# Optimization experiments

Hardware: AMD Instinct MI355X
Metric: run time of the kernel (lower is better)

The kernel has to match this reference:

```python
import jax, jax.numpy as jnp
import numpy as np

B, T, E, H = 8, 2048, 1024, 64  # batch, seq_len(=block_size), embedding_size, head_size


def setup_inputs() -> dict:
    key = jax.random.key(0)
    k1, k2, k3, k4, k5 = jax.random.split(key, 5)
    x = jax.random.normal(k1, (B, T, E), dtype=jnp.float32)
    Wk = jax.random.normal(k2, (H, E), dtype=jnp.float32) * 0.02
    Wq = jax.random.normal(k3, (H, E), dtype=jnp.float32) * 0.02
    Wv = jax.random.normal(k4, (H, E), dtype=jnp.float32) * 0.02
    attention_mask = jax.random.randint(k5, (B, T), 0, 2).astype(jnp.int32)
    return {"x": x, "Wk": Wk, "Wq": Wq, "Wv": Wv, "attention_mask": attention_mask}


def reference(x, Wk, Wq, Wv, attention_mask):
    # Linear projections (nn.Linear with no bias: y = x @ W.T)
    k = jnp.einsum('bte,he->bth', x, Wk)
    q = jnp.einsum('bte,he->bth', x, Wq)
    v = jnp.einsum('bte,he->bth', x, Wv)
    scale = v.shape[2] ** -0.5  # head_size^-0.5, faithful to v.shape[2]**(-0.5)
    wei = jnp.einsum('bqh,bkh->bqk', q, k) * scale  # [B,T,T]
    # Causal mask (tril buffer) AND padding outer-product mask; the double-precision
    # outer product in the original just tests nonzero-ness, so a boolean AND is exact.
    causal = jnp.tril(jnp.ones((T, T), dtype=bool))  # [T,T]
    pad = (attention_mask[:, :, None] * attention_mask[:, None, :]) != 0  # [B,T,T]
    wei = jnp.where(causal[None, :, :] & pad, wei, -jnp.inf)
    wei = jax.nn.softmax(wei, axis=-1)
    wei = jnp.nan_to_num(wei)  # fully-masked rows -> 0 (matches torch.nan_to_num)
    # dropout in eval mode -> identity
    out = jnp.einsum('bqk,bkh->bqh', wei, v)
    return out
```

## Files before the change

### kernel.cpp

```cpp
#include <hip/hip_runtime.h>
#include <hip/hip_bf16.h>

typedef __bf16 bf16x8 __attribute__((ext_vector_type(8)));
typedef __bf16 bf16x4 __attribute__((ext_vector_type(4)));
typedef float  f32x4  __attribute__((ext_vector_type(4)));

#define LDP  72
#define KLDP 72
#define VLDP 72
#define PLDP 72

#define BAR() { asm volatile("s_waitcnt lgkmcnt(0)" ::: "memory"); __builtin_amdgcn_s_barrier(); }

__global__ __launch_bounds__(256) void wconv_kernel(
    const float* __restrict__ Wk, const float* __restrict__ Wq,
    const float* __restrict__ Wv, const int* __restrict__ mask,
    __bf16* __restrict__ wbf, unsigned* __restrict__ maskw)
{
    if (blockIdx.x == 192) {
        for (int wdx = threadIdx.x; wdx < 512; wdx += 256) {
            unsigned wv = 0;
            #pragma unroll
            for (int bit = 0; bit < 32; bit++)
                wv |= (mask[wdx * 32 + bit] != 0 ? 1u : 0u) << bit;
            maskw[wdx] = wv;
        }
        return;
    }
    int idx = blockIdx.x * 256 + threadIdx.x;
    int row = idx >> 8;
    int c4  = idx & 255;
    const float* wp = (row < 64) ? Wk + (size_t)row * 1024
                    : (row < 128) ? Wq + (size_t)(row - 64) * 1024
                                  : Wv + (size_t)(row - 128) * 1024;
    float4 f = *reinterpret_cast<const float4*>(wp + c4 * 4);
    bf16x4 v; v[0] = (__bf16)f.x; v[1] = (__bf16)f.y; v[2] = (__bf16)f.z; v[3] = (__bf16)f.w;
    *reinterpret_cast<bf16x4*>(&wbf[(size_t)row * 1024 + c4 * 4]) = v;
}

__global__ __launch_bounds__(1024) void proj_kernel(
    const float* __restrict__ x, const __bf16* __restrict__ wbf,
    __bf16* __restrict__ kbuf, __bf16* __restrict__ qbuf, __bf16* __restrict__ vtbuf)
{
    __shared__ __align__(16) __bf16 Slds[2][256 * LDP];
    __shared__ __align__(16) __bf16 Vtl[64 * LDP];

    const int tid  = threadIdx.x;
    const int lane = tid & 63;
    const int wid  = tid >> 6;
    const int wm   = wid >> 2;
    const int wn   = wid & 3;
    const int mbase = blockIdx.x * 64;

    const int cl = lane & 15;
    const int e0 = (lane >> 4) * 8;
    const int r0 = (lane >> 4) * 4;

    const int arow = tid >> 4, acg = tid & 15;
    const float* aptr = x + (size_t)(mbase + arow) * 1024 + acg * 4;

    float4 a0, a1;
    bf16x4 w0[3], w1[3];

#define ISSUE(aset, wset, kb) { \
    aset = *reinterpret_cast<const float4*>(aptr + (kb)); \
    _Pragma("unroll") \
    for (int i_ = 0; i_ < 3; i_++) { \
        int c_ = i_ * 1024 + tid; \
        wset[i_] = *reinterpret_cast<const bf16x4*>(&wbf[(size_t)(c_ >> 4) * 1024 + (kb) + (c_ & 15) * 4]); \
    } }

#define COMMIT(aset, wset, bufi) { \
    bf16x4 av_; \
    av_[0] = (__bf16)aset.x; av_[1] = (__bf16)aset.y; av_[2] = (__bf16)aset.z; av_[3] = (__bf16)aset.w; \
    *reinterpret_cast<bf16x4*>(&Slds[bufi][arow * LDP + acg * 4]) = av_; \
    _Pragma("unroll") \
    for (int i_ = 0; i_ < 3; i_++) { \
        int c_ = i_ * 1024 + tid; \
        *reinterpret_cast<bf16x4*>(&Slds[bufi][(64 + (c_ >> 4)) * LDP + (c_ & 15) * 4]) = wset[i_]; \
    } }

    f32x4 acc[3];
    #pragma unroll
    for (int n = 0; n < 3; n++) acc[n] = (f32x4){0.f, 0.f, 0.f, 0.f};

    ISSUE(a0, w0, 0);
    COMMIT(a0, w0, 0);
    ISSUE(a1, w1, 64);
    BAR();

    #pragma unroll 2
    for (int j = 0; j < 16; j++) {
        if (j < 14) {
            if (j & 1) { ISSUE(a1, w1, (j + 2) * 64); }
            else       { ISSUE(a0, w0, (j + 2) * 64); }
        }
        const __bf16* buf = Slds[j & 1];
        #pragma unroll
        for (int kk = 0; kk < 2; kk++) {
            bf16x8 a = *reinterpret_cast<const bf16x8*>(&buf[(wm * 16 + cl) * LDP + kk * 32 + e0]);
            #pragma unroll
            for (int nf = 0; nf < 3; nf++) {
                bf16x8 b = *reinterpret_cast<const bf16x8*>(&buf[(64 + wn * 48 + nf * 16 + cl) * LDP + kk * 32 + e0]);
                acc[nf] = __builtin_amdgcn_mfma_f32_16x16x32_bf16(a, b, acc[nf], 0, 0, 0);
            }
        }
        if (j < 15) {
            if (j & 1) { COMMIT(a0, w0, 0); }
            else       { COMMIT(a1, w1, 1); }
            BAR();
        }
    }
#undef ISSUE
#undef COMMIT

    #pragma unroll
    for (int nf = 0; nf < 3; nf++) {
        int c = wn * 48 + nf * 16 + cl;
        #pragma unroll
        for (int r = 0; r < 4; r++) {
            int mrel = wm * 16 + r0 + r;
            float v = acc[nf][r];
            if (c < 64)        kbuf[(size_t)(mbase + mrel) * 64 + c]         = (__bf16)v;
            else if (c < 128)  qbuf[(size_t)(mbase + mrel) * 64 + (c - 64)]  = (__bf16)v;
            else               Vtl[(c - 128) * LDP + mrel]                   = (__bf16)v;
        }
    }
    __syncthreads();
    {
        int b   = mbase >> 11;
        int tof = mbase & 2047;
        int h   = tid >> 4;
        int seg = tid & 15;
        bf16x4 v4 = *reinterpret_cast<const bf16x4*>(&Vtl[h * LDP + seg * 4]);
        *reinterpret_cast<bf16x4*>(&vtbuf[(size_t)b * 64 * 2048 + (size_t)h * 2048 + tof + seg * 4]) = v4;
    }
}

__global__ __launch_bounds__(128) void attn_kernel(
    const __bf16* __restrict__ qbuf, const __bf16* __restrict__ kbuf,
    const __bf16* __restrict__ vtbuf, const unsigned* __restrict__ maskw,
    float* __restrict__ out, float* __restrict__ accpart, float* __restrict__ mlpart,
    int nsplit, int tps)
{
    __shared__ __align__(16) __bf16 Klds[64 * KLDP];
    __shared__ __align__(16) __bf16 Vlds[64 * VLDP];
    __shared__ __align__(16) __bf16 Plds[2][2][16 * PLDP];

    const int tid  = threadIdx.x;
    const int lane = tid & 63;
    const int w    = tid >> 6;
    const int wg   = blockIdx.x;
    const int b    = wg & 7;
    const int rr_  = wg >> 3;
    const int qt   = rr_ & 31;
    const int sp   = rr_ >> 5;

    const int jbeg = sp * tps;
    const int jend = min((sp + 1) * tps, qt + 1);

    if (nsplit > 1 && jbeg >= jend) {
        for (int i = tid; i < 64; i += 128) {
            size_t mo = ((size_t)(b * nsplit + sp) * 2048 + qt * 64 + i) * 2;
            mlpart[mo] = -INFINITY; mlpart[mo + 1] = 0.f;
        }
        return;
    }

    const int cl = lane & 15;
    const int e0 = (lane >> 4) * 8;
    const int r0 = (lane >> 4) * 4;
    const int qs0 = qt * 64 + w * 16 + cl;
    const int qs1 = qs0 + 32;

    bf16x8 aq0[2], aq1[2];
    #pragma unroll
    for (int kk = 0; kk < 2; kk++) {
        aq0[kk] = *reinterpret_cast<const bf16x8*>(&qbuf[((size_t)b * 2048 + qs0) * 64 + kk * 32 + e0]);
        aq1[kk] = *reinterpret_cast<const bf16x8*>(&qbuf[((size_t)b * 2048 + qs1) * 64 + kk * 32 + e0]);
    }

    float m0 = -INFINITY, l0 = 0.f, m1 = -INFINITY, l1 = 0.f;
    f32x4 acc0[4], acc1[4];
    #pragma unroll
    for (int hf = 0; hf < 4; hf++) { acc0[hf] = (f32x4){0.f,0.f,0.f,0.f}; acc1[hf] = (f32x4){0.f,0.f,0.f,0.f}; }

    const __bf16* kb  = kbuf  + (size_t)b * 2048 * 64;
    const __bf16* vtb = vtbuf + (size_t)b * 64 * 2048;

    const int srow = tid >> 1;
    const int sc   = (tid & 1) * 32;
    bf16x8 stk[4], stv[4];

#define KV_ISSUE(jj) { _Pragma("unroll") for (int i_ = 0; i_ < 4; i_++) { \
    stk[i_] = *reinterpret_cast<const bf16x8*>(&kb[(size_t)((jj) * 64 + srow) * 64 + sc + i_ * 8]); \
    stv[i_] = *reinterpret_cast<const bf16x8*>(&vtb[(size_t)srow * 2048 + (jj) * 64 + sc + i_ * 8]); } }

#define KV_COMMIT() { _Pragma("unroll") for (int i_ = 0; i_ < 4; i_++) { \
    *reinterpret_cast<bf16x8*>(&Klds[srow * KLDP + sc + i_ * 8]) = stk[i_]; \
    *reinterpret_cast<bf16x8*>(&Vlds[srow * VLDP + sc + i_ * 8]) = stv[i_]; } }

#define SOFTMAX(S, mS, lS, accS, qsS, su) { \
    float tmax = -INFINITY; \
    _Pragma("unroll") for (int jf = 0; jf < 4; jf++) { \
        unsigned mw = (jf < 2) ? mw0 : mw1; \
        _Pragma("unroll") for (int r = 0; r < 4; r++) { \
            int kvl = jf * 16 + r0 + r; \
            bool ok = ((mw >> (kvl & 31)) & 1u) && (j * 64 + kvl <= qsS); \
            float sv = S[jf][r] * 0.125f; \
            sv = ok ? sv : -INFINITY; \
            S[jf][r] = sv; tmax = fmaxf(tmax, sv); } } \
    tmax = fmaxf(tmax, __shfl_xor(tmax, 16)); \
    tmax = fmaxf(tmax, __shfl_xor(tmax, 32)); \
    float mn = fmaxf(mS, tmax); \
    float alpha = (mn == -INFINITY) ? 1.0f : __expf(mS - mn); \
    float rs = 0.f; \
    _Pragma("unroll") for (int jf = 0; jf < 4; jf++) \
        _Pragma("unroll") for (int r = 0; r < 4; r++) { \
            float p = (mn == -INFINITY) ? 0.f : __expf(S[jf][r] - mn); \
            S[jf][r] = p; rs += p; } \
    rs += __shfl_xor(rs, 16); \
    rs += __shfl_xor(rs, 32); \
    lS = lS * alpha + rs; mS = mn; \
    _Pragma("unroll") for (int hf = 0; hf < 4; hf++) \
        _Pragma("unroll") for (int r = 0; r < 4; r++) accS[hf][r] *= alpha; \
    _Pragma("unroll") for (int jf = 0; jf < 4; jf++) { \
        bf16x4 p4; \
        _Pragma("unroll") for (int r = 0; r < 4; r++) p4[r] = (__bf16)S[jf][r]; \
        *reinterpret_cast<bf16x4*>(&Plds[w][su][cl * PLDP + jf * 16 + r0]) = p4; } }

    const int nt = jend - jbeg;
    KV_ISSUE(jbeg);
    KV_COMMIT();
    if (nt > 1) KV_ISSUE(jbeg + 1);
    BAR();

    for (int t = 0; t < nt; t++) {
        const int j = jbeg + t;

        f32x4 s0[4], s1[4];
        #pragma unroll
        for (int jf = 0; jf < 4; jf++) {
            f32x4 t0 = (f32x4){0.f,0.f,0.f,0.f}, t1 = (f32x4){0.f,0.f,0.f,0.f};
            #pragma unroll
            for (int kk = 0; kk < 2; kk++) {
                bf16x8 bk = *reinterpret_cast<const bf16x8*>(&Klds[(jf * 16 + cl) * KLDP + kk * 32 + e0]);
                t0 = __builtin_amdgcn_mfma_f32_16x16x32_bf16(bk, aq0[kk], t0, 0, 0, 0);
                t1 = __builtin_amdgcn_mfma_f32_16x16x32_bf16(bk, aq1[kk], t1, 0, 0, 0);
            }
            s0[jf] = t0; s1[jf] = t1;
        }

        const unsigned mw0 = maskw[b * 64 + j * 2];
        const unsigned mw1 = maskw[b * 64 + j * 2 + 1];
        SOFTMAX(s0, m0, l0, acc0, qs0, 0);
        SOFTMAX(s1, m1, l1, acc1, qs1, 1);

        #pragma unroll
        for (int kk = 0; kk < 2; kk++) {
            bf16x8 p0 = *reinterpret_cast<const bf16x8*>(&Plds[w][0][cl * PLDP + kk * 32 + e0]);
            bf16x8 p1 = *reinterpret_cast<const bf16x8*>(&Plds[w][1][cl * PLDP + kk * 32 + e0]);
            #pragma unroll
            for (int hf = 0; hf < 4; hf++) {
                bf16x8 av = *reinterpret_cast<const bf16x8*>(&Vlds[(hf * 16 + cl) * VLDP + kk * 32 + e0]);
                acc0[hf] = __builtin_amdgcn_mfma_f32_16x16x32_bf16(av, p0, acc0[hf], 0, 0, 0);
                acc1[hf] = __builtin_amdgcn_mfma_f32_16x16x32_bf16(av, p1, acc1[hf], 0, 0, 0);
            }
        }

        BAR();
        if (t + 1 < nt) {
            KV_COMMIT();
            if (t + 2 < nt) KV_ISSUE(j + 2);
            BAR();
        }
    }
#undef KV_ISSUE
#undef KV_COMMIT
#undef SOFTMAX

    const bool mq0 = (maskw[b * 64 + (qs0 >> 5)] >> (qs0 & 31)) & 1u;
    const bool mq1 = (maskw[b * 64 + (qs1 >> 5)] >> (qs1 & 31)) & 1u;
    if (nsplit == 1) {
        #pragma unroll
        for (int hf = 0; hf < 4; hf++)
            #pragma unroll
            for (int r = 0; r < 4; r++) {
                float v0 = (l0 > 0.f && mq0) ? acc0[hf][r] / l0 : 0.f;
                float v1 = (l1 > 0.f && mq1) ? acc1[hf][r] / l1 : 0.f;
                out[((size_t)b * 2048 + qs0) * 64 + hf * 16 + r0 + r] = v0;
                out[((size_t)b * 2048 + qs1) * 64 + hf * 16 + r0 + r] = v1;
            }
    } else {
        #pragma unroll
        for (int hf = 0; hf < 4; hf++)
            #pragma unroll
            for (int r = 0; r < 4; r++) {
                accpart[((size_t)(b * nsplit + sp) * 2048 + qs0) * 64 + hf * 16 + r0 + r] = acc0[hf][r];
                accpart[((size_t)(b * nsplit + sp) * 2048 + qs1) * 64 + hf * 16 + r0 + r] = acc1[hf][r];
            }
        if (lane < 16) {
            size_t mo0 = ((size_t)(b * nsplit + sp) * 2048 + qs0) * 2;
            size_t mo1 = ((size_t)(b * nsplit + sp) * 2048 + qs1) * 2;
            mlpart[mo0] = m0; mlpart[mo0 + 1] = l0;
            mlpart[mo1] = m1; mlpart[mo1 + 1] = l1;
        }
    }
}

template<int NS>
__global__ __launch_bounds__(256) void combine_kernel(
    const float* __restrict__ accpart, const float* __restrict__ mlpart,
    const unsigned* __restrict__ maskw, float* __restrict__ out)
{
    int idx = blockIdx.x * 256 + threadIdx.x;
    int qglob = idx >> 6;
    int h = idx & 63;
    int b = qglob >> 11;
    int qrow = qglob & 2047;

    if (!((maskw[b * 64 + (qrow >> 5)] >> (qrow & 31)) & 1u)) { out[idx] = 0.f; return; }

    float m_s[NS], l_s[NS];
    float M = -INFINITY;
    #pragma unroll
    for (int s = 0; s < NS; s++) {
        size_t mo = ((size_t)(b * NS + s) * 2048 + qrow) * 2;
        m_s[s] = mlpart[mo];
        l_s[s] = mlpart[mo + 1];
        M = fmaxf(M, m_s[s]);
    }
    if (M == -INFINITY) { out[idx] = 0.f; return; }

    float L = 0.f, O = 0.f;
    #pragma unroll
    for (int s = 0; s < NS; s++) {
        float wgt = (m_s[s] == -INFINITY) ? 0.f : __expf(m_s[s] - M);
        L += l_s[s] * wgt;
        O += wgt * accpart[((size_t)(b * NS + s) * 2048 + qrow) * 64 + h];
    }
    out[idx] = (L > 0.f) ? O / L : 0.f;
}

extern "C" void kernel_launch(void* const* d_in, const int* in_sizes, int n_in,
                              void* d_out, int out_size, void* d_ws, size_t ws_size,
                              hipStream_t stream) {
    const float* x  = (const float*)d_in[0];
    const float* Wk = (const float*)d_in[1];
    const float* Wq = (const float*)d_in[2];
    const float* Wv = (const float*)d_in[3];
    const int* mask = (const int*)d_in[4];
    float* out = (float*)d_out;

    const size_t NTOK = 8 * 2048;
    __bf16* kbuf  = (__bf16*)d_ws;
    __bf16* qbuf  = kbuf + NTOK * 64;
    __bf16* vtbuf = qbuf + NTOK * 64;
    __bf16* wbf   = vtbuf + (size_t)8 * 64 * 2048;
    unsigned* maskw = (unsigned*)(wbf + (size_t)192 * 1024);
    const size_t base_bytes = NTOK * 64 * 2 * 2 + (size_t)8 * 64 * 2048 * 2
                            + (size_t)192 * 1024 * 2 + 512 * 4;

    const size_t acc_per_split = NTOK * 64 * 4;
    const size_t ml_per_split  = NTOK * 2 * 4;
    int nsplit = 1;
    if (ws_size >= base_bytes + 4 * (acc_per_split + ml_per_split))      nsplit = 4;
    else if (ws_size >= base_bytes + 2 * (acc_per_split + ml_per_split)) nsplit = 2;

    float* accpart = (float*)((char*)d_ws + base_bytes);
    float* mlpart  = accpart + NTOK * 64 * nsplit;

    wconv_kernel<<<193, 256, 0, stream>>>(Wk, Wq, Wv, mask, wbf, maskw);
    proj_kernel<<<256, 1024, 0, stream>>>(x, wbf, kbuf, qbuf, vtbuf);
    attn_kernel<<<8 * 32 * nsplit, 128, 0, stream>>>(
        qbuf, kbuf, vtbuf, maskw, out, accpart, mlpart, nsplit, 32 / nsplit);
    if (nsplit == 4)
        combine_kernel<4><<<(16384 * 64) / 256, 256, 0, stream>>>(accpart, mlpart, maskw, out);
    else if (nsplit == 2)
        combine_kernel<2><<<(16384 * 64) / 256, 256, 0, stream>>>(accpart, mlpart, maskw, out);
}
```

Measured before the change: 58.21 us.

## Load projection weights directly into registers and halve proj block size

The projection kernel now works on 32-token tiles with 512 threads and 512 blocks instead of 64 tokens with 1024 threads. Each wave loads its weight fragments straight from global memory into registers, and the weight tile no longer goes through LDS. This removes LDS write/read traffic and shrinks shared memory, so more blocks can run at once. The cost is more global weight loads per token, because each block re-reads the full weight slice for half as many rows, and higher register use. The combine kernel also skips the accpart load for splits that are fully masked.

```diff
diff --git a/kernel.cpp b/kernel.cpp
--- a/kernel.cpp
+++ b/kernel.cpp
@@ -6,6 +6,7 @@
 typedef float  f32x4  __attribute__((ext_vector_type(4)));
 
 #define LDP  72
+#define VTP  40
 #define KLDP 72
 #define VLDP 72
 #define PLDP 72
@@ -38,19 +39,19 @@
     *reinterpret_cast<bf16x4*>(&wbf[(size_t)row * 1024 + c4 * 4]) = v;
 }
 
-__global__ __launch_bounds__(1024) void proj_kernel(
+__global__ __launch_bounds__(512) void proj_kernel(
     const float* __restrict__ x, const __bf16* __restrict__ wbf,
     __bf16* __restrict__ kbuf, __bf16* __restrict__ qbuf, __bf16* __restrict__ vtbuf)
 {
-    __shared__ __align__(16) __bf16 Slds[2][256 * LDP];
-    __shared__ __align__(16) __bf16 Vtl[64 * LDP];
+    __shared__ __align__(16) __bf16 Alds[2][32 * LDP];
+    __shared__ __align__(16) __bf16 Vtl[64 * VTP];
 
     const int tid  = threadIdx.x;
     const int lane = tid & 63;
     const int wid  = tid >> 6;
     const int wm   = wid >> 2;
     const int wn   = wid & 3;
-    const int mbase = blockIdx.x * 64;
+    const int mbase = blockIdx.x * 32;
 
     const int cl = lane & 15;
     const int e0 = (lane >> 4) * 8;
@@ -58,61 +59,52 @@
 
     const int arow = tid >> 4, acg = tid & 15;
     const float* aptr = x + (size_t)(mbase + arow) * 1024 + acg * 4;
+    const __bf16* wptr = wbf + (size_t)(wn * 48) * 1024;
 
     float4 a0, a1;
-    bf16x4 w0[3], w1[3];
-
-#define ISSUE(aset, wset, kb) { \
-    aset = *reinterpret_cast<const float4*>(aptr + (kb)); \
-    _Pragma("unroll") \
-    for (int i_ = 0; i_ < 3; i_++) { \
-        int c_ = i_ * 1024 + tid; \
-        wset[i_] = *reinterpret_cast<const bf16x4*>(&wbf[(size_t)(c_ >> 4) * 1024 + (kb) + (c_ & 15) * 4]); \
-    } }
-
-#define COMMIT(aset, wset, bufi) { \
-    bf16x4 av_; \
+    bf16x8 w0[6], w1[6];
+
+#define ISSUE_A(aset, kb) { aset = *reinterpret_cast<const float4*>(aptr + (kb)); }
+#define ISSUE_W(wset, kb) { _Pragma("unroll") for (int f_ = 0; f_ < 6; f_++) { \
+    int nf_ = f_ >> 1, kk_ = f_ & 1; \
+    wset[f_] = *reinterpret_cast<const bf16x8*>(&wptr[(size_t)(nf_ * 16 + cl) * 1024 + (kb) + kk_ * 32 + e0]); } }
+#define COMMIT_A(aset, bufi) { bf16x4 av_; \
     av_[0] = (__bf16)aset.x; av_[1] = (__bf16)aset.y; av_[2] = (__bf16)aset.z; av_[3] = (__bf16)aset.w; \
-    *reinterpret_cast<bf16x4*>(&Slds[bufi][arow * LDP + acg * 4]) = av_; \
-    _Pragma("unroll") \
-    for (int i_ = 0; i_ < 3; i_++) { \
-        int c_ = i_ * 1024 + tid; \
-        *reinterpret_cast<bf16x4*>(&Slds[bufi][(64 + (c_ >> 4)) * LDP + (c_ & 15) * 4]) = wset[i_]; \
-    } }
+    *reinterpret_cast<bf16x4*>(&Alds[bufi][arow * LDP + acg * 4]) = av_; }
 
     f32x4 acc[3];
     #pragma unroll
     for (int n = 0; n < 3; n++) acc[n] = (f32x4){0.f, 0.f, 0.f, 0.f};
 
-    ISSUE(a0, w0, 0);
-    COMMIT(a0, w0, 0);
-    ISSUE(a1, w1, 64);
+    ISSUE_A(a0, 0); COMMIT_A(a0, 0); ISSUE_W(w0, 0);
+    ISSUE_A(a1, 64); ISSUE_W(w1, 64);
     BAR();
 
     #pragma unroll 2
     for (int j = 0; j < 16; j++) {
-        if (j < 14) {
-            if (j & 1) { ISSUE(a1, w1, (j + 2) * 64); }
-            else       { ISSUE(a0, w0, (j + 2) * 64); }
-        }
-        const __bf16* buf = Slds[j & 1];
+        const __bf16* abuf = Alds[j & 1];
         #pragma unroll
         for (int kk = 0; kk < 2; kk++) {
-            bf16x8 a = *reinterpret_cast<const bf16x8*>(&buf[(wm * 16 + cl) * LDP + kk * 32 + e0]);
+            bf16x8 a = *reinterpret_cast<const bf16x8*>(&abuf[(wm * 16 + cl) * LDP + kk * 32 + e0]);
             #pragma unroll
             for (int nf = 0; nf < 3; nf++) {
-                bf16x8 b = *reinterpret_cast<const bf16x8*>(&buf[(64 + wn * 48 + nf * 16 + cl) * LDP + kk * 32 + e0]);
-                acc[nf] = __builtin_amdgcn_mfma_f32_16x16x32_bf16(a, b, acc[nf], 0, 0, 0);
+                if (j & 1) acc[nf] = __builtin_amdgcn_mfma_f32_16x16x32_bf16(a, w1[nf * 2 + kk], acc[nf], 0, 0, 0);
+                else       acc[nf] = __builtin_amdgcn_mfma_f32_16x16x32_bf16(a, w0[nf * 2 + kk], acc[nf], 0, 0, 0);
             }
         }
         if (j < 15) {
-            if (j & 1) { COMMIT(a0, w0, 0); }
-            else       { COMMIT(a1, w1, 1); }
+            if (j & 1) { COMMIT_A(a0, 0); }
+            else       { COMMIT_A(a1, 1); }
+            if (j < 14) {
+                if (j & 1) { ISSUE_A(a1, (j + 2) * 64); ISSUE_W(w1, (j + 2) * 64); }
+                else       { ISSUE_A(a0, (j + 2) * 64); ISSUE_W(w0, (j + 2) * 64); }
+            }
             BAR();
         }
     }
-#undef ISSUE
-#undef COMMIT
+#undef ISSUE_A
+#undef ISSUE_W
+#undef COMMIT_A
 
     #pragma unroll
     for (int nf = 0; nf < 3; nf++) {
@@ -123,16 +115,16 @@
             float v = acc[nf][r];
             if (c < 64)        kbuf[(size_t)(mbase + mrel) * 64 + c]         = (__bf16)v;
             else if (c < 128)  qbuf[(size_t)(mbase + mrel) * 64 + (c - 64)]  = (__bf16)v;
-            else               Vtl[(c - 128) * LDP + mrel]                   = (__bf16)v;
+            else               Vtl[(c - 128) * VTP + mrel]                   = (__bf16)v;
         }
     }
     __syncthreads();
     {
         int b   = mbase >> 11;
         int tof = mbase & 2047;
-        int h   = tid >> 4;
-        int seg = tid & 15;
-        bf16x4 v4 = *reinterpret_cast<const bf16x4*>(&Vtl[h * LDP + seg * 4]);
+        int h   = tid >> 3;
+        int seg = tid & 7;
+        bf16x4 v4 = *reinterpret_cast<const bf16x4*>(&Vtl[h * VTP + seg * 4]);
         *reinterpret_cast<bf16x4*>(&vtbuf[(size_t)b * 64 * 2048 + (size_t)h * 2048 + tof + seg * 4]) = v4;
     }
 }
@@ -335,9 +327,11 @@
     float L = 0.f, O = 0.f;
     #pragma unroll
     for (int s = 0; s < NS; s++) {
-        float wgt = (m_s[s] == -INFINITY) ? 0.f : __expf(m_s[s] - M);
-        L += l_s[s] * wgt;
-        O += wgt * accpart[((size_t)(b * NS + s) * 2048 + qrow) * 64 + h];
+        if (m_s[s] > -INFINITY) {
+            float wgt = __expf(m_s[s] - M);
+            L += l_s[s] * wgt;
+            O += wgt * accpart[((size_t)(b * NS + s) * 2048 + qrow) * 64 + h];
+        }
     }
     out[idx] = (L > 0.f) ? O / L : 0.f;
 }
@@ -371,7 +365,7 @@
     float* mlpart  = accpart + NTOK * 64 * nsplit;
 
     wconv_kernel<<<193, 256, 0, stream>>>(Wk, Wq, Wv, mask, wbf, maskw);
-    proj_kernel<<<256, 1024, 0, stream>>>(x, wbf, kbuf, qbuf, vtbuf);
+    proj_kernel<<<512, 512, 0, stream>>>(x, wbf, kbuf, qbuf, vtbuf);
     attn_kernel<<<8 * 32 * nsplit, 128, 0, stream>>>(
         qbuf, kbuf, vtbuf, maskw, out, accpart, mlpart, nsplit, 32 / nsplit);
     if (nsplit == 4)
```

Result: slower. 89.76 us (+54.2%).
